# Performance work log

Measured on AMD Instinct MI355X. Metric: run time of the kernel, lower is better.

The kernel has to match this reference:

```python
import jax, jax.numpy as jnp
import numpy as np

ROPE_THETA = 10000.0
NUM_HEADS = 16


def _apply_rope(t, positions):
    # t: [B, H, S, dh]; positions: [S] int
    dh = t.shape[-1]
    inv_freq = 1.0 / (ROPE_THETA ** (jnp.arange(0, dh, 2, dtype=jnp.float32) / dh))  # [dh/2]
    ang = positions.astype(jnp.float32)[:, None] * inv_freq[None, :]  # [S, dh/2]
    cos = jnp.cos(ang)[None, None]  # [1,1,S,dh/2]
    sin = jnp.sin(ang)[None, None]
    t1 = t[..., 0::2]
    t2 = t[..., 1::2]
    r1 = t1 * cos - t2 * sin
    r2 = t1 * sin + t2 * cos
    # interleave back: (r1_0, r2_0, r1_1, r2_1, ...)
    return jnp.stack([r1, r2], axis=-1).reshape(t.shape)


def setup_inputs() -> dict:
    key = jax.random.key(0)
    ks = jax.random.split(key, 5)
    B, S, D = 4, 2048, 1024
    sigma = np.sqrt(2.0 / (D + D))
    return {
        "x": jax.random.normal(ks[0], (B, S, D), dtype=jnp.float32),
        "WQ": jax.random.normal(ks[1], (D, D), dtype=jnp.float32) * sigma,
        "WK": jax.random.normal(ks[2], (D, D), dtype=jnp.float32) * sigma,
        "WV": jax.random.normal(ks[3], (D, D), dtype=jnp.float32) * sigma,
        "WO": jax.random.normal(ks[4], (D, D), dtype=jnp.float32) * sigma,
        "token_positions": jnp.arange(S, dtype=jnp.int32),
    }


def reference(x, WQ, WK, WV, WO, token_positions):
    B, S, D = x.shape
    H = NUM_HEADS
    dh = D // H

    def proj(W):
        # x @ W.T, then split heads -> [B, H, S, dh]
        return jnp.einsum('bsd,ed->bse', x, W).reshape(B, S, H, dh).transpose(0, 2, 1, 3)

    Q = _apply_rope(proj(WQ), token_positions)
    K = _apply_rope(proj(WK), token_positions)
    V = proj(WV)

    scale = 1.0 / jnp.sqrt(jnp.asarray(dh, dtype=x.dtype))
    scores = jnp.einsum('bhqd,bhkd->bhqk', Q, K) * scale  # [B,H,S,S]
    causal = jnp.tril(jnp.ones((S, S), dtype=bool))
    scores = jnp.where(causal[None, None], scores, jnp.asarray(-jnp.inf, dtype=scores.dtype))
    attn = jax.nn.softmax(scores, axis=-1)
    out = jnp.einsum('bhqk,bhkd->bhqd', attn, V)  # [B,H,S,dh]
    out = out.transpose(0, 2, 1, 3).reshape(B, S, D)
    return out @ WO.T
```

## Files before the change

### kernel.cpp

```cpp
#include <hip/hip_runtime.h>
#include <hip/hip_bf16.h>
#include <math.h>

constexpr int NB   = 4;
constexpr int SEQ  = 2048;
constexpr int DM   = 1024;
constexpr int NH   = 16;
constexpr int DH2  = 64;
constexpr int NROWS = NB * SEQ;

typedef __attribute__((ext_vector_type(8))) short bf16x8;
typedef __attribute__((ext_vector_type(4))) short bf16x4;
typedef __attribute__((ext_vector_type(4))) float f32x4;

__device__ __forceinline__ unsigned short f2bf(float f) {
  __hip_bfloat16 h = __float2bfloat16(f);
  return *reinterpret_cast<unsigned short*>(&h);
}

__device__ __forceinline__ f32x4 mfma16(bf16x8 a, bf16x8 b, f32x4 c) {
  return __builtin_amdgcn_mfma_f32_16x16x32_bf16(a, b, c, 0, 0, 0);
}

__device__ __forceinline__ f32x4 mfma16k16(bf16x4 a, bf16x4 b, f32x4 c) {
  asm("v_mfma_f32_16x16x16_bf16 %0, %1, %2, %0" : "+v"(c) : "v"(a), "v"(b));
  return c;
}

__device__ __forceinline__ void gload_lds16(const void* g, void* l) {
  __builtin_amdgcn_global_load_lds(
      (const __attribute__((address_space(1))) void*)g,
      (__attribute__((address_space(3))) void*)l, 16, 0, 0);
}

__global__ void cast_kernel(const float* __restrict__ in,
                            unsigned short* __restrict__ out, int n4) {
  int i = blockIdx.x * blockDim.x + threadIdx.x;
  int stride = gridDim.x * blockDim.x;
  for (int idx = i; idx < n4; idx += stride) {
    float4 v = reinterpret_cast<const float4*>(in)[idx];
    ushort4 o;
    o.x = f2bf(v.x); o.y = f2bf(v.y); o.z = f2bf(v.z); o.w = f2bf(v.w);
    reinterpret_cast<ushort4*>(out)[idx] = o;
  }
}

__global__ void rope_table_kernel(float2* __restrict__ tab, const int* __restrict__ pos) {
  int idx = blockIdx.x * blockDim.x + threadIdx.x;
  if (idx >= SEQ * 32) return;
  int s = idx >> 5, i = idx & 31;
  float inv = powf(10000.0f, -(float)i * (1.0f / 32.0f));
  float ang = (float)pos[s] * inv;
  tab[idx] = make_float2(cosf(ang), sinf(ang));
}

template<int MODE>
__global__ __launch_bounds__(256)
void gemm_bt(const unsigned short* __restrict__ Ag,
             const unsigned short* __restrict__ Bg,
             void* __restrict__ Cout,
             const float2* __restrict__ tab)
{
  constexpr int K = DM;
  __shared__ unsigned short As[128 * 32];
  __shared__ unsigned short Bs[128 * 32];
  const int tid = threadIdx.x;
  const int w = tid >> 6, lane = tid & 63;
  const int wr = w >> 1, wc = w & 1;
  const int r = lane & 15, g = lane >> 4;
  const int rowTile = blockIdx.x, colTile = blockIdx.y;
  const unsigned short* Abase = Ag + (size_t)rowTile * 128 * K;
  const unsigned short* Bbase = Bg + (size_t)colTile * 128 * K;

  f32x4 acc[4][4];
#pragma unroll
  for (int m = 0; m < 4; ++m)
#pragma unroll
    for (int n = 0; n < 4; ++n) acc[m][n] = f32x4{0.f, 0.f, 0.f, 0.f};

  const int e0 = w * 1024 + lane * 8;

  for (int k0 = 0; k0 < K; k0 += 32) {
#pragma unroll
    for (int c = 0; c < 2; ++c) {
      int e = e0 + c * 512;
      int trow = e >> 5, tcol = e & 31;
      gload_lds16(Abase + (size_t)trow * K + k0 + tcol, As + (w * 2 + c) * 512);
      gload_lds16(Bbase + (size_t)trow * K + k0 + tcol, Bs + (w * 2 + c) * 512);
    }
    __syncthreads();
    bf16x8 a[4], b[4];
#pragma unroll
    for (int m = 0; m < 4; ++m)
      a[m] = *reinterpret_cast<const bf16x8*>(As + (wr * 64 + m * 16 + r) * 32 + g * 8);
#pragma unroll
    for (int n = 0; n < 4; ++n)
      b[n] = *reinterpret_cast<const bf16x8*>(Bs + (wc * 64 + n * 16 + r) * 32 + g * 8);
#pragma unroll
    for (int m = 0; m < 4; ++m)
#pragma unroll
      for (int n = 0; n < 4; ++n)
        acc[m][n] = mfma16(a[m], b[n], acc[m][n]);
    __syncthreads();
  }

  const int row0 = rowTile * 128 + wr * 64;
  const int col0 = colTile * 128 + wc * 64;
  if constexpr (MODE == 0) {
    float* C = reinterpret_cast<float*>(Cout);
#pragma unroll
    for (int m = 0; m < 4; ++m)
#pragma unroll
      for (int n = 0; n < 4; ++n)
#pragma unroll
        for (int j = 0; j < 4; ++j) {
          int rr = row0 + m * 16 + g * 4 + j;
          int cc = col0 + n * 16 + r;
          C[(size_t)rr * DM + cc] = acc[m][n][j];
        }
  } else {
    unsigned short* Ob = reinterpret_cast<unsigned short*>(Cout);
#pragma unroll
    for (int m = 0; m < 4; ++m)
#pragma unroll
      for (int n = 0; n < 4; ++n)
#pragma unroll
        for (int j = 0; j < 4; ++j) {
          int rr = row0 + m * 16 + g * 4 + j;
          int ee = col0 + n * 16 + r;
          float val = acc[m][n][j];
          if constexpr (MODE == 1) {
            float partner = __shfl_xor(val, 1);
            int dd = ee & 63;
            int sr = rr & (SEQ - 1);
            float2 cs = tab[sr * 32 + (dd >> 1)];
            val = val * cs.x + (((ee & 1) == 0) ? -partner : partner) * cs.y;
          }
          int bb = rr >> 11;
          int sr2 = rr & (SEQ - 1);
          int h = ee >> 6, d = ee & 63;
          Ob[((size_t)(bb * NH + h) * SEQ + sr2) * DH2 + d] = f2bf(val);
        }
  }
}

__global__ __launch_bounds__(256)
void flash_attn(const unsigned short* __restrict__ Qb,
                const unsigned short* __restrict__ Kb,
                const unsigned short* __restrict__ Vb,
                unsigned short* __restrict__ AO)
{
  constexpr int VST = 68;
  __shared__ unsigned short Vt[2][64 * VST];
  const int tid = threadIdx.x;
  const int w = tid >> 6, lane = tid & 63;
  const int r = lane & 15, g = lane >> 4;
  const int pr = blockIdx.x;
  const int bh = blockIdx.y;
  const unsigned short* Qh = Qb + (size_t)bh * SEQ * DH2;
  const unsigned short* Kh = Kb + (size_t)bh * SEQ * DH2;
  const unsigned short* Vh = Vb + (size_t)bh * SEQ * DH2;
  const int bb = bh >> 4, h = bh & 15;
  const int vd  = (lane & 7) * 8;
  const int vkv = w * 16 + (lane >> 3) * 2;
  const float C = 0.18033688f;
  const float NEG_INF = -__builtin_inff();

  for (int ctx = 0; ctx < 2; ++ctx) {
    const int qt = ctx ? pr : (15 - pr);
    const int q0w = qt * 128 + w * 32;
    const int nT  = 2 * qt + 2;
    const int myT = 2 * qt + 1 + (w >> 1);

    bf16x8 qf[2][2];
#pragma unroll
    for (int mq = 0; mq < 2; ++mq)
#pragma unroll
      for (int kk = 0; kk < 2; ++kk)
        qf[mq][kk] = *reinterpret_cast<const bf16x8*>(
            Qh + (size_t)(q0w + mq * 16 + r) * DH2 + kk * 32 + g * 8);

    bf16x8 kc[2][4], kn[2][4];
#pragma unroll
    for (int kk = 0; kk < 2; ++kk)
#pragma unroll
      for (int nk = 0; nk < 4; ++nk)
        kc[kk][nk] = *reinterpret_cast<const bf16x8*>(
            Kh + (size_t)(nk * 16 + r) * DH2 + kk * 32 + g * 8);

    {
      bf16x8 a0 = *reinterpret_cast<const bf16x8*>(Vh + (size_t)vkv * DH2 + vd);
      bf16x8 a1 = *reinterpret_cast<const bf16x8*>(Vh + (size_t)(vkv + 1) * DH2 + vd);
#pragma unroll
      for (int dd = 0; dd < 8; ++dd) {
        unsigned int pk = (unsigned int)(unsigned short)a0[dd] |
                          ((unsigned int)(unsigned short)a1[dd] << 16);
        *reinterpret_cast<unsigned int*>(&Vt[0][(vd + dd) * VST + vkv]) = pk;
      }
    }
    __syncthreads();

    f32x4 oacc[2][4];
    float m_run[2], l_part[2];
#pragma unroll
    for (int mq = 0; mq < 2; ++mq) {
#pragma unroll
      for (int nd = 0; nd < 4; ++nd) oacc[mq][nd] = f32x4{0.f, 0.f, 0.f, 0.f};
      m_run[mq] = NEG_INF;
      l_part[mq] = 0.f;
    }

    bf16x8 va0, va1;
    for (int t = 0; t < nT; ++t) {
      const int cur = t & 1;
      const int tn = (t + 1 < nT) ? (t + 1) : t;
      const size_t kv0n = (size_t)tn * 64;

#pragma unroll
      for (int kk = 0; kk < 2; ++kk)
#pragma unroll
        for (int nk = 0; nk < 4; ++nk)
          kn[kk][nk] = *reinterpret_cast<const bf16x8*>(
              Kh + (kv0n + nk * 16 + r) * DH2 + kk * 32 + g * 8);
      va0 = *reinterpret_cast<const bf16x8*>(Vh + (kv0n + vkv) * DH2 + vd);
      va1 = *reinterpret_cast<const bf16x8*>(Vh + (kv0n + vkv + 1) * DH2 + vd);

      if (t < myT) {
        const int kv0 = t * 64;
        f32x4 sacc[2][4];
#pragma unroll
        for (int mq = 0; mq < 2; ++mq)
#pragma unroll
          for (int nk = 0; nk < 4; ++nk) sacc[mq][nk] = f32x4{0.f, 0.f, 0.f, 0.f};
        __builtin_amdgcn_s_setprio(1);
#pragma unroll
        for (int kk = 0; kk < 2; ++kk)
#pragma unroll
          for (int mq = 0; mq < 2; ++mq)
#pragma unroll
            for (int nk = 0; nk < 4; ++nk)
              sacc[mq][nk] = mfma16(kc[kk][nk], qf[mq][kk], sacc[mq][nk]);
        __builtin_amdgcn_s_setprio(0);

        if (t == myT - 1) {
#pragma unroll
          for (int mq = 0; mq < 2; ++mq) {
            const int qg = q0w + mq * 16 + r;
#pragma unroll
            for (int nk = 0; nk < 4; ++nk)
#pragma unroll
              for (int j = 0; j < 4; ++j) {
                int kg = kv0 + nk * 16 + g * 4 + j;
                if (kg > qg) sacc[mq][nk][j] = NEG_INF;
              }
          }
        }

        float vmax[2];
#pragma unroll
        for (int mq = 0; mq < 2; ++mq) {
          float v0 = fmaxf(fmaxf(sacc[mq][0][0], sacc[mq][0][1]),
                           fmaxf(sacc[mq][0][2], sacc[mq][0][3]));
          float v1 = fmaxf(fmaxf(sacc[mq][1][0], sacc[mq][1][1]),
                           fmaxf(sacc[mq][1][2], sacc[mq][1][3]));
          float v2 = fmaxf(fmaxf(sacc[mq][2][0], sacc[mq][2][1]),
                           fmaxf(sacc[mq][2][2], sacc[mq][2][3]));
          float v3 = fmaxf(fmaxf(sacc[mq][3][0], sacc[mq][3][1]),
                           fmaxf(sacc[mq][3][2], sacc[mq][3][3]));
          float v = fmaxf(fmaxf(v0, v1), fmaxf(v2, v3));
          v = fmaxf(v, __shfl_xor(v, 16));
          v = fmaxf(v, __shfl_xor(v, 32));
          vmax[mq] = v;
        }

        int cskip = (vmax[0] <= m_run[0] + 64.f) && (vmax[1] <= m_run[1] + 64.f);
        if (!__all(cskip)) {
#pragma unroll
          for (int mq = 0; mq < 2; ++mq) {
            float mo = m_run[mq];
            float mn = fmaxf(mo, vmax[mq]);
            float cr = exp2f((mo - mn) * C);
            m_run[mq] = mn;
            l_part[mq] *= cr;
            float co[4];
#pragma unroll
            for (int j = 0; j < 4; ++j) co[j] = __shfl(cr, g * 4 + j);
#pragma unroll
            for (int nd = 0; nd < 4; ++nd)
#pragma unroll
              for (int j = 0; j < 4; ++j)
                oacc[mq][nd][j] *= co[j];
          }
        }

        bf16x4 pa[2][4];
#pragma unroll
        for (int mq = 0; mq < 2; ++mq) {
          float mC = m_run[mq] * C;
          float ls = 0.f;
#pragma unroll
          for (int nk = 0; nk < 4; ++nk) {
            float p0 = exp2f(fmaf(sacc[mq][nk][0], C, -mC));
            float p1 = exp2f(fmaf(sacc[mq][nk][1], C, -mC));
            float p2 = exp2f(fmaf(sacc[mq][nk][2], C, -mC));
            float p3 = exp2f(fmaf(sacc[mq][nk][3], C, -mC));
            ls += (p0 + p1) + (p2 + p3);
            pa[mq][nk] = bf16x4{(short)f2bf(p0), (short)f2bf(p1),
                                (short)f2bf(p2), (short)f2bf(p3)};
          }
          l_part[mq] += ls;
        }

        __builtin_amdgcn_s_setprio(1);
#pragma unroll
        for (int nd = 0; nd < 4; ++nd) {
          bf16x4 vb[4];
#pragma unroll
          for (int nk = 0; nk < 4; ++nk)
            vb[nk] = *reinterpret_cast<const bf16x4*>(
                &Vt[cur][(nd * 16 + r) * VST + nk * 16 + 4 * g]);
#pragma unroll
          for (int mq = 0; mq < 2; ++mq)
#pragma unroll
            for (int nk = 0; nk < 4; ++nk)
              oacc[mq][nd] = mfma16k16(pa[mq][nk], vb[nk], oacc[mq][nd]);
        }
        __builtin_amdgcn_s_setprio(0);
      }

#pragma unroll
      for (int dd = 0; dd < 8; ++dd) {
        unsigned int pk = (unsigned int)(unsigned short)va0[dd] |
                          ((unsigned int)(unsigned short)va1[dd] << 16);
        *reinterpret_cast<unsigned int*>(&Vt[cur ^ 1][(vd + dd) * VST + vkv]) = pk;
      }
#pragma unroll
      for (int kk = 0; kk < 2; ++kk)
#pragma unroll
        for (int nk = 0; nk < 4; ++nk) kc[kk][nk] = kn[kk][nk];
      __syncthreads();
    }

#pragma unroll
    for (int mq = 0; mq < 2; ++mq) {
      float l = l_part[mq];
      l += __shfl_xor(l, 16);
      l += __shfl_xor(l, 32);
#pragma unroll
      for (int j = 0; j < 4; ++j) {
        float inv = 1.0f / __shfl(l, g * 4 + j);
        int srow = q0w + mq * 16 + g * 4 + j;
#pragma unroll
        for (int nd = 0; nd < 4; ++nd) {
          int d = nd * 16 + r;
          AO[(size_t)(bb * SEQ + srow) * DM + h * DH2 + d] = f2bf(oacc[mq][nd][j] * inv);
        }
      }
    }
  }
}

extern "C" void kernel_launch(void* const* d_in, const int* in_sizes, int n_in,
                              void* d_out, int out_size, void* d_ws, size_t ws_size,
                              hipStream_t stream) {
  const float* x  = (const float*)d_in[0];
  const float* WQ = (const float*)d_in[1];
  const float* WK = (const float*)d_in[2];
  const float* WV = (const float*)d_in[3];
  const float* WO = (const float*)d_in[4];
  const int* pos  = (const int*)d_in[5];

  char* ws = (char*)d_ws;
  unsigned short* xb  = (unsigned short*)(ws + 0);
  unsigned short* wqb = (unsigned short*)(ws + (16u << 20));
  unsigned short* wkb = (unsigned short*)(ws + (18u << 20));
  unsigned short* wvb = (unsigned short*)(ws + (20u << 20));
  unsigned short* wob = (unsigned short*)(ws + (22u << 20));
  unsigned short* Qb  = (unsigned short*)(ws + (24u << 20));
  unsigned short* Kb  = (unsigned short*)(ws + (40u << 20));
  unsigned short* Vb  = (unsigned short*)(ws + (56u << 20));
  unsigned short* AO  = (unsigned short*)(ws + (72u << 20));
  float2* tab = (float2*)(ws + (88u << 20));

  cast_kernel<<<2048, 256, 0, stream>>>(x, xb, NROWS * DM / 4);
  cast_kernel<<<256, 256, 0, stream>>>(WQ, wqb, DM * DM / 4);
  cast_kernel<<<256, 256, 0, stream>>>(WK, wkb, DM * DM / 4);
  cast_kernel<<<256, 256, 0, stream>>>(WV, wvb, DM * DM / 4);
  cast_kernel<<<256, 256, 0, stream>>>(WO, wob, DM * DM / 4);
  rope_table_kernel<<<(SEQ * 32 + 255) / 256, 256, 0, stream>>>(tab, pos);

  dim3 gproj(NROWS / 128, DM / 128);
  gemm_bt<1><<<gproj, 256, 0, stream>>>(xb, wqb, (void*)Qb, tab);
  gemm_bt<1><<<gproj, 256, 0, stream>>>(xb, wkb, (void*)Kb, tab);
  gemm_bt<2><<<gproj, 256, 0, stream>>>(xb, wvb, (void*)Vb, nullptr);
  flash_attn<<<dim3(8, NB * NH), 256, 0, stream>>>(Qb, Kb, Vb, AO);
  gemm_bt<0><<<gproj, 256, 0, stream>>>(AO, wob, d_out, nullptr);
}
```

Before: 228.1 us.

## Split paired query tiles into separate blocks and ping-pong K registers

Each attention block now handles one query tile instead of a balanced pair, so the grid doubles to 16×64 blocks. Heavier tiles are placed first to help load balance. The KV loop is unrolled by two with alternating K register buffers, which removes the per-iteration register copy. V transposition into LDS now uses byte-permute instructions, and exp2 calls use the hardware builtin. The trade-off is losing the pairwise causal load balancing within a block and possibly different register pressure.

```diff
diff --git a/kernel.cpp b/kernel.cpp
--- a/kernel.cpp
+++ b/kernel.cpp
@@ -155,7 +155,7 @@
   const int tid = threadIdx.x;
   const int w = tid >> 6, lane = tid & 63;
   const int r = lane & 15, g = lane >> 4;
-  const int pr = blockIdx.x;
+  const int qt = 15 - blockIdx.x;
   const int bh = blockIdx.y;
   const unsigned short* Qh = Qb + (size_t)bh * SEQ * DH2;
   const unsigned short* Kh = Kb + (size_t)bh * SEQ * DH2;
@@ -166,195 +166,209 @@
   const float C = 0.18033688f;
   const float NEG_INF = -__builtin_inff();
 
-  for (int ctx = 0; ctx < 2; ++ctx) {
-    const int qt = ctx ? pr : (15 - pr);
-    const int q0w = qt * 128 + w * 32;
-    const int nT  = 2 * qt + 2;
-    const int myT = 2 * qt + 1 + (w >> 1);
-
-    bf16x8 qf[2][2];
+  const int q0w = qt * 128 + w * 32;
+  const int nT  = 2 * qt + 2;
+  const int myT = 2 * qt + 1 + (w >> 1);
+
+  bf16x8 qf[2][2];
+#pragma unroll
+  for (int mq = 0; mq < 2; ++mq)
+#pragma unroll
+    for (int kk = 0; kk < 2; ++kk)
+      qf[mq][kk] = *reinterpret_cast<const bf16x8*>(
+          Qh + (size_t)(q0w + mq * 16 + r) * DH2 + kk * 32 + g * 8);
+
+  bf16x8 kA[2][4], kB[2][4];
+#pragma unroll
+  for (int kk = 0; kk < 2; ++kk)
+#pragma unroll
+    for (int nk = 0; nk < 4; ++nk)
+      kA[kk][nk] = *reinterpret_cast<const bf16x8*>(
+          Kh + (size_t)(nk * 16 + r) * DH2 + kk * 32 + g * 8);
+
+  {
+    const uint4* p0 = reinterpret_cast<const uint4*>(Vh + (size_t)vkv * DH2 + vd);
+    const uint4* p1 = reinterpret_cast<const uint4*>(Vh + (size_t)(vkv + 1) * DH2 + vd);
+    uint4 a0 = *p0, a1 = *p1;
+    const unsigned int* d0 = reinterpret_cast<const unsigned int*>(&a0);
+    const unsigned int* d1 = reinterpret_cast<const unsigned int*>(&a1);
+#pragma unroll
+    for (int k2 = 0; k2 < 4; ++k2) {
+      *reinterpret_cast<unsigned int*>(&Vt[0][(vd + 2 * k2) * VST + vkv]) =
+          __builtin_amdgcn_perm(d1[k2], d0[k2], 0x05040100u);
+      *reinterpret_cast<unsigned int*>(&Vt[0][(vd + 2 * k2 + 1) * VST + vkv]) =
+          __builtin_amdgcn_perm(d1[k2], d0[k2], 0x07060302u);
+    }
+  }
+  __syncthreads();
+
+  f32x4 oacc[2][4];
+  float m_run[2], l_part[2];
+#pragma unroll
+  for (int mq = 0; mq < 2; ++mq) {
+#pragma unroll
+    for (int nd = 0; nd < 4; ++nd) oacc[mq][nd] = f32x4{0.f, 0.f, 0.f, 0.f};
+    m_run[mq] = NEG_INF;
+    l_part[mq] = 0.f;
+  }
+
+  uint4 va0, va1;
+
+  auto prefetchK = [&](int tile, bf16x8 (&kf)[2][4]) {
+    const size_t kv0n = (size_t)tile * 64;
+#pragma unroll
+    for (int kk = 0; kk < 2; ++kk)
+#pragma unroll
+      for (int nk = 0; nk < 4; ++nk)
+        kf[kk][nk] = *reinterpret_cast<const bf16x8*>(
+            Kh + (kv0n + nk * 16 + r) * DH2 + kk * 32 + g * 8);
+  };
+  auto prefetchV = [&](int tile) {
+    const size_t kv0n = (size_t)tile * 64;
+    va0 = *reinterpret_cast<const uint4*>(Vh + (kv0n + vkv) * DH2 + vd);
+    va1 = *reinterpret_cast<const uint4*>(Vh + (kv0n + vkv + 1) * DH2 + vd);
+  };
+  auto stageV = [&](int buf) {
+    const unsigned int* d0 = reinterpret_cast<const unsigned int*>(&va0);
+    const unsigned int* d1 = reinterpret_cast<const unsigned int*>(&va1);
+#pragma unroll
+    for (int k2 = 0; k2 < 4; ++k2) {
+      *reinterpret_cast<unsigned int*>(&Vt[buf][(vd + 2 * k2) * VST + vkv]) =
+          __builtin_amdgcn_perm(d1[k2], d0[k2], 0x05040100u);
+      *reinterpret_cast<unsigned int*>(&Vt[buf][(vd + 2 * k2 + 1) * VST + vkv]) =
+          __builtin_amdgcn_perm(d1[k2], d0[k2], 0x07060302u);
+    }
+  };
+
+  auto computeTile = [&](int t, bf16x8 (&kf)[2][4], int cur) {
+    const int kv0 = t * 64;
+    f32x4 sacc[2][4];
 #pragma unroll
     for (int mq = 0; mq < 2; ++mq)
 #pragma unroll
-      for (int kk = 0; kk < 2; ++kk)
-        qf[mq][kk] = *reinterpret_cast<const bf16x8*>(
-            Qh + (size_t)(q0w + mq * 16 + r) * DH2 + kk * 32 + g * 8);
-
-    bf16x8 kc[2][4], kn[2][4];
+      for (int nk = 0; nk < 4; ++nk) sacc[mq][nk] = f32x4{0.f, 0.f, 0.f, 0.f};
+    __builtin_amdgcn_s_setprio(1);
 #pragma unroll
     for (int kk = 0; kk < 2; ++kk)
 #pragma unroll
+      for (int mq = 0; mq < 2; ++mq)
+#pragma unroll
+        for (int nk = 0; nk < 4; ++nk)
+          sacc[mq][nk] = mfma16(kf[kk][nk], qf[mq][kk], sacc[mq][nk]);
+    __builtin_amdgcn_s_setprio(0);
+
+    if (t == myT - 1) {
+#pragma unroll
+      for (int mq = 0; mq < 2; ++mq) {
+        const int qg = q0w + mq * 16 + r;
+#pragma unroll
+        for (int nk = 0; nk < 4; ++nk)
+#pragma unroll
+          for (int j = 0; j < 4; ++j) {
+            int kg = kv0 + nk * 16 + g * 4 + j;
+            if (kg > qg) sacc[mq][nk][j] = NEG_INF;
+          }
+      }
+    }
+
+    float vmax[2];
+#pragma unroll
+    for (int mq = 0; mq < 2; ++mq) {
+      float v0 = fmaxf(fmaxf(sacc[mq][0][0], sacc[mq][0][1]),
+                       fmaxf(sacc[mq][0][2], sacc[mq][0][3]));
+      float v1 = fmaxf(fmaxf(sacc[mq][1][0], sacc[mq][1][1]),
+                       fmaxf(sacc[mq][1][2], sacc[mq][1][3]));
+      float v2 = fmaxf(fmaxf(sacc[mq][2][0], sacc[mq][2][1]),
+                       fmaxf(sacc[mq][2][2], sacc[mq][2][3]));
+      float v3 = fmaxf(fmaxf(sacc[mq][3][0], sacc[mq][3][1]),
+                       fmaxf(sacc[mq][3][2], sacc[mq][3][3]));
+      float v = fmaxf(fmaxf(v0, v1), fmaxf(v2, v3));
+      v = fmaxf(v, __shfl_xor(v, 16));
+      v = fmaxf(v, __shfl_xor(v, 32));
+      vmax[mq] = v;
+    }
+
+    int cskip = (vmax[0] <= m_run[0] + 64.f) && (vmax[1] <= m_run[1] + 64.f);
+    if (!__all(cskip)) {
+#pragma unroll
+      for (int mq = 0; mq < 2; ++mq) {
+        float mo = m_run[mq];
+        float mn = fmaxf(mo, vmax[mq]);
+        float cr = __builtin_amdgcn_exp2f((mo - mn) * C);
+        m_run[mq] = mn;
+        l_part[mq] *= cr;
+        float co[4];
+#pragma unroll
+        for (int j = 0; j < 4; ++j) co[j] = __shfl(cr, g * 4 + j);
+#pragma unroll
+        for (int nd = 0; nd < 4; ++nd)
+#pragma unroll
+          for (int j = 0; j < 4; ++j)
+            oacc[mq][nd][j] *= co[j];
+      }
+    }
+
+    bf16x4 pa[2][4];
+#pragma unroll
+    for (int mq = 0; mq < 2; ++mq) {
+      float mC = m_run[mq] * C;
+      float ls = 0.f;
+#pragma unroll
+      for (int nk = 0; nk < 4; ++nk) {
+        float p0 = __builtin_amdgcn_exp2f(fmaf(sacc[mq][nk][0], C, -mC));
+        float p1 = __builtin_amdgcn_exp2f(fmaf(sacc[mq][nk][1], C, -mC));
+        float p2 = __builtin_amdgcn_exp2f(fmaf(sacc[mq][nk][2], C, -mC));
+        float p3 = __builtin_amdgcn_exp2f(fmaf(sacc[mq][nk][3], C, -mC));
+        ls += (p0 + p1) + (p2 + p3);
+        pa[mq][nk] = bf16x4{(short)f2bf(p0), (short)f2bf(p1),
+                            (short)f2bf(p2), (short)f2bf(p3)};
+      }
+      l_part[mq] += ls;
+    }
+
+    __builtin_amdgcn_s_setprio(1);
+#pragma unroll
+    for (int nd = 0; nd < 4; ++nd) {
+      bf16x4 vb[4];
+#pragma unroll
       for (int nk = 0; nk < 4; ++nk)
-        kc[kk][nk] = *reinterpret_cast<const bf16x8*>(
-            Kh + (size_t)(nk * 16 + r) * DH2 + kk * 32 + g * 8);
-
-    {
-      bf16x8 a0 = *reinterpret_cast<const bf16x8*>(Vh + (size_t)vkv * DH2 + vd);
-      bf16x8 a1 = *reinterpret_cast<const bf16x8*>(Vh + (size_t)(vkv + 1) * DH2 + vd);
-#pragma unroll
-      for (int dd = 0; dd < 8; ++dd) {
-        unsigned int pk = (unsigned int)(unsigned short)a0[dd] |
-                          ((unsigned int)(unsigned short)a1[dd] << 16);
-        *reinterpret_cast<unsigned int*>(&Vt[0][(vd + dd) * VST + vkv]) = pk;
-      }
-    }
+        vb[nk] = *reinterpret_cast<const bf16x4*>(
+            &Vt[cur][(nd * 16 + r) * VST + nk * 16 + 4 * g]);
+#pragma unroll
+      for (int mq = 0; mq < 2; ++mq)
+#pragma unroll
+        for (int nk = 0; nk < 4; ++nk)
+          oacc[mq][nd] = mfma16k16(pa[mq][nk], vb[nk], oacc[mq][nd]);
+    }
+    __builtin_amdgcn_s_setprio(0);
+  };
+
+  for (int t = 0; t < nT; t += 2) {
+    prefetchK((t + 1 < nT) ? t + 1 : nT - 1, kB);
+    prefetchV((t + 1 < nT) ? t + 1 : nT - 1);
+    if (t < myT) computeTile(t, kA, 0);
+    stageV(1);
     __syncthreads();
-
-    f32x4 oacc[2][4];
-    float m_run[2], l_part[2];
-#pragma unroll
-    for (int mq = 0; mq < 2; ++mq) {
-#pragma unroll
-      for (int nd = 0; nd < 4; ++nd) oacc[mq][nd] = f32x4{0.f, 0.f, 0.f, 0.f};
-      m_run[mq] = NEG_INF;
-      l_part[mq] = 0.f;
-    }
-
-    bf16x8 va0, va1;
-    for (int t = 0; t < nT; ++t) {
-      const int cur = t & 1;
-      const int tn = (t + 1 < nT) ? (t + 1) : t;
-      const size_t kv0n = (size_t)tn * 64;
-
-#pragma unroll
-      for (int kk = 0; kk < 2; ++kk)
-#pragma unroll
-        for (int nk = 0; nk < 4; ++nk)
-          kn[kk][nk] = *reinterpret_cast<const bf16x8*>(
-              Kh + (kv0n + nk * 16 + r) * DH2 + kk * 32 + g * 8);
-      va0 = *reinterpret_cast<const bf16x8*>(Vh + (kv0n + vkv) * DH2 + vd);
-      va1 = *reinterpret_cast<const bf16x8*>(Vh + (kv0n + vkv + 1) * DH2 + vd);
-
-      if (t < myT) {
-        const int kv0 = t * 64;
-        f32x4 sacc[2][4];
-#pragma unroll
-        for (int mq = 0; mq < 2; ++mq)
-#pragma unroll
-          for (int nk = 0; nk < 4; ++nk) sacc[mq][nk] = f32x4{0.f, 0.f, 0.f, 0.f};
-        __builtin_amdgcn_s_setprio(1);
-#pragma unroll
-        for (int kk = 0; kk < 2; ++kk)
-#pragma unroll
-          for (int mq = 0; mq < 2; ++mq)
-#pragma unroll
-            for (int nk = 0; nk < 4; ++nk)
-              sacc[mq][nk] = mfma16(kc[kk][nk], qf[mq][kk], sacc[mq][nk]);
-        __builtin_amdgcn_s_setprio(0);
-
-        if (t == myT - 1) {
-#pragma unroll
-          for (int mq = 0; mq < 2; ++mq) {
-            const int qg = q0w + mq * 16 + r;
-#pragma unroll
-            for (int nk = 0; nk < 4; ++nk)
-#pragma unroll
-              for (int j = 0; j < 4; ++j) {
-                int kg = kv0 + nk * 16 + g * 4 + j;
-                if (kg > qg) sacc[mq][nk][j] = NEG_INF;
-              }
-          }
-        }
-
-        float vmax[2];
-#pragma unroll
-        for (int mq = 0; mq < 2; ++mq) {
-          float v0 = fmaxf(fmaxf(sacc[mq][0][0], sacc[mq][0][1]),
-                           fmaxf(sacc[mq][0][2], sacc[mq][0][3]));
-          float v1 = fmaxf(fmaxf(sacc[mq][1][0], sacc[mq][1][1]),
-                           fmaxf(sacc[mq][1][2], sacc[mq][1][3]));
-          float v2 = fmaxf(fmaxf(sacc[mq][2][0], sacc[mq][2][1]),
-                           fmaxf(sacc[mq][2][2], sacc[mq][2][3]));
-          float v3 = fmaxf(fmaxf(sacc[mq][3][0], sacc[mq][3][1]),
-                           fmaxf(sacc[mq][3][2], sacc[mq][3][3]));
-          float v = fmaxf(fmaxf(v0, v1), fmaxf(v2, v3));
-          v = fmaxf(v, __shfl_xor(v, 16));
-          v = fmaxf(v, __shfl_xor(v, 32));
-          vmax[mq] = v;
-        }
-
-        int cskip = (vmax[0] <= m_run[0] + 64.f) && (vmax[1] <= m_run[1] + 64.f);
-        if (!__all(cskip)) {
-#pragma unroll
-          for (int mq = 0; mq < 2; ++mq) {
-            float mo = m_run[mq];
-            float mn = fmaxf(mo, vmax[mq]);
-            float cr = exp2f((mo - mn) * C);
-            m_run[mq] = mn;
-            l_part[mq] *= cr;
-            float co[4];
-#pragma unroll
-            for (int j = 0; j < 4; ++j) co[j] = __shfl(cr, g * 4 + j);
-#pragma unroll
-            for (int nd = 0; nd < 4; ++nd)
-#pragma unroll
-              for (int j = 0; j < 4; ++j)
-                oacc[mq][nd][j] *= co[j];
-          }
-        }
-
-        bf16x4 pa[2][4];
-#pragma unroll
-        for (int mq = 0; mq < 2; ++mq) {
-          float mC = m_run[mq] * C;
-          float ls = 0.f;
-#pragma unroll
-          for (int nk = 0; nk < 4; ++nk) {
-            float p0 = exp2f(fmaf(sacc[mq][nk][0], C, -mC));
-            float p1 = exp2f(fmaf(sacc[mq][nk][1], C, -mC));
-            float p2 = exp2f(fmaf(sacc[mq][nk][2], C, -mC));
-            float p3 = exp2f(fmaf(sacc[mq][nk][3], C, -mC));
-            ls += (p0 + p1) + (p2 + p3);
-            pa[mq][nk] = bf16x4{(short)f2bf(p0), (short)f2bf(p1),
-                                (short)f2bf(p2), (short)f2bf(p3)};
-          }
-          l_part[mq] += ls;
-        }
-
-        __builtin_amdgcn_s_setprio(1);
-#pragma unroll
-        for (int nd = 0; nd < 4; ++nd) {
-          bf16x4 vb[4];
-#pragma unroll
-          for (int nk = 0; nk < 4; ++nk)
-            vb[nk] = *reinterpret_cast<const bf16x4*>(
-                &Vt[cur][(nd * 16 + r) * VST + nk * 16 + 4 * g]);
-#pragma unroll
-          for (int mq = 0; mq < 2; ++mq)
-#pragma unroll
-            for (int nk = 0; nk < 4; ++nk)
-              oacc[mq][nd] = mfma16k16(pa[mq][nk], vb[nk], oacc[mq][nd]);
-        }
-        __builtin_amdgcn_s_setprio(0);
-      }
-
-#pragma unroll
-      for (int dd = 0; dd < 8; ++dd) {
-        unsigned int pk = (unsigned int)(unsigned short)va0[dd] |
-                          ((unsigned int)(unsigned short)va1[dd] << 16);
-        *reinterpret_cast<unsigned int*>(&Vt[cur ^ 1][(vd + dd) * VST + vkv]) = pk;
-      }
-#pragma unroll
-      for (int kk = 0; kk < 2; ++kk)
-#pragma unroll
-        for (int nk = 0; nk < 4; ++nk) kc[kk][nk] = kn[kk][nk];
-      __syncthreads();
-    }
-
-#pragma unroll
-    for (int mq = 0; mq < 2; ++mq) {
-      float l = l_part[mq];
-      l += __shfl_xor(l, 16);
-      l += __shfl_xor(l, 32);
-#pragma unroll
-      for (int j = 0; j < 4; ++j) {
-        float inv = 1.0f / __shfl(l, g * 4 + j);
-        int srow = q0w + mq * 16 + g * 4 + j;
-#pragma unroll
-        for (int nd = 0; nd < 4; ++nd) {
-          int d = nd * 16 + r;
-          AO[(size_t)(bb * SEQ + srow) * DM + h * DH2 + d] = f2bf(oacc[mq][nd][j] * inv);
-        }
+    prefetchK((t + 2 < nT) ? t + 2 : nT - 1, kA);
+    prefetchV((t + 2 < nT) ? t + 2 : nT - 1);
+    if (t + 1 < myT) computeTile(t + 1, kB, 1);
+    stageV(0);
+    __syncthreads();
+  }
+
+#pragma unroll
+  for (int mq = 0; mq < 2; ++mq) {
+    float l = l_part[mq];
+    l += __shfl_xor(l, 16);
+    l += __shfl_xor(l, 32);
+#pragma unroll
+    for (int j = 0; j < 4; ++j) {
+      float inv = 1.0f / __shfl(l, g * 4 + j);
+      int srow = q0w + mq * 16 + g * 4 + j;
+#pragma unroll
+      for (int nd = 0; nd < 4; ++nd) {
+        int d = nd * 16 + r;
+        AO[(size_t)(bb * SEQ + srow) * DM + h * DH2 + d] = f2bf(oacc[mq][nd][j] * inv);
       }
     }
   }
@@ -393,6 +407,6 @@
   gemm_bt<1><<<gproj, 256, 0, stream>>>(xb, wqb, (void*)Qb, tab);
   gemm_bt<1><<<gproj, 256, 0, stream>>>(xb, wkb, (void*)Kb, tab);
   gemm_bt<2><<<gproj, 256, 0, stream>>>(xb, wvb, (void*)Vb, nullptr);
-  flash_attn<<<dim3(8, NB * NH), 256, 0, stream>>>(Qb, Kb, Vb, AO);
+  flash_attn<<<dim3(16, NB * NH), 256, 0, stream>>>(Qb, Kb, Vb, AO);
   gemm_bt<0><<<gproj, 256, 0, stream>>>(AO, wob, d_out, nullptr);
 }
```

After: 266.1 us. 1.17x slower.
